# Optimization experiments

Measured on AMD Instinct MI355X. Metric: run time of the kernel, lower is better.

Reference implementation:

```python
import jax, jax.numpy as jnp
import numpy as np

B, T, F = 131072, 15, 12
H1, H2, CS = 64, 128, 96  # num_h1, num_h2, input_feature*8


def _lstm_cell(x, h, c, w_ih, w_hh, b_ih, b_hh):
    # torch.nn.LSTMCell gate order: i, f, g, o
    gates = x @ w_ih.T + h @ w_hh.T + b_ih + b_hh  # [B, 4H]
    i, f, g, o = jnp.split(gates, 4, axis=-1)
    i, f, o = jax.nn.sigmoid(i), jax.nn.sigmoid(f), jax.nn.sigmoid(o)
    g = jnp.tanh(g)
    c_new = f * c + i * g
    h_new = o * jnp.tanh(c_new)
    return h_new, c_new


def setup_inputs() -> dict:
    key = jax.random.key(0)
    ks = jax.random.split(key, 16)
    s = 0.05
    return {
        "input_seq": jax.random.normal(ks[0], (B, T, F), jnp.float32),
        "cell_state": jax.random.normal(ks[1], (B, CS), jnp.float32),
        "fc1_w": jax.random.normal(ks[2], (H1, CS), jnp.float32) * s,
        "fc1_b": jnp.zeros((H1,), jnp.float32),
        "fc2_w": jax.random.normal(ks[3], (H2, CS), jnp.float32) * s,
        "fc2_b": jnp.zeros((H2,), jnp.float32),
        "l0_w_ih": jax.random.normal(ks[4], (4 * H1, F), jnp.float32) * s,
        "l0_w_hh": jax.random.normal(ks[5], (4 * H1, H1), jnp.float32) * s,
        "l0_b_ih": jnp.zeros((4 * H1,), jnp.float32),
        "l0_b_hh": jnp.zeros((4 * H1,), jnp.float32),
        "l1_w_ih": jax.random.normal(ks[6], (4 * H2, H1), jnp.float32) * s,
        "l1_w_hh": jax.random.normal(ks[7], (4 * H2, H2), jnp.float32) * s,
        "l1_b_ih": jnp.zeros((4 * H2,), jnp.float32),
        "l1_b_hh": jnp.zeros((4 * H2,), jnp.float32),
        "d1_w": jax.random.normal(ks[8], (H1, H2), jnp.float32) * s,
        "d1_b": jnp.zeros((H1,), jnp.float32),
        "d2_w": jax.random.normal(ks[9], (1, H1), jnp.float32) * s,
        "d2_b": jnp.zeros((1,), jnp.float32),
    }


def reference(input_seq, cell_state, fc1_w, fc1_b, fc2_w, fc2_b,
              l0_w_ih, l0_w_hh, l0_b_ih, l0_b_hh,
              l1_w_ih, l1_w_hh, l1_b_ih, l1_b_hh,
              d1_w, d1_b, d2_w, d2_b):
    # dropout in eval mode (identity) for deterministic reference
    h0 = jnp.zeros((input_seq.shape[0], H1), input_seq.dtype)
    c0 = cell_state @ fc1_w.T + fc1_b
    h1 = jnp.zeros((input_seq.shape[0], H2), input_seq.dtype)
    c1 = cell_state @ fc2_w.T + fc2_b

    def step(carry, x_t):
        h0, c0, h1, c1 = carry
        h0n, c0_res = _lstm_cell(x_t, h0, c0, l0_w_ih, l0_w_hh, l0_b_ih, l0_b_hh)
        c0n = c0 + c0_res  # residual cell state
        h1n, c1_res = _lstm_cell(h0n, h1, c1, l1_w_ih, l1_w_hh, l1_b_ih, l1_b_hh)
        c1n = c1 + c1_res
        return (h0n, c0n, h1n, c1n), None

    xs = jnp.swapaxes(input_seq, 0, 1)  # [T, B, F]
    (h0, c0, h1, c1), _ = jax.lax.scan(step, (h0, c0, h1, c1), xs)
    pred = (h1 @ d1_w.T + d1_b) @ d2_w.T + d2_b  # [B, 1]
    return pred
```

## Files before the change

kernel.cpp:

```cpp
#include <hip/hip_runtime.h>


typedef float    f32x4 __attribute__((ext_vector_type(4)));
typedef _Float16 f16x8 __attribute__((ext_vector_type(8)));
typedef _Float16 f16x4 __attribute__((ext_vector_type(4)));

#define DEV static __device__ __forceinline__

DEV float fexp2(float x){ return __builtin_amdgcn_exp2f(x); }
DEV float frcp (float x){ return __builtin_amdgcn_rcpf(x); }

#define MFMA16(A,B,C) __builtin_amdgcn_mfma_f32_16x16x32_f16(A,B,C,0,0,0)

constexpr int T = 15, F = 12, CS = 96;
constexpr int R = 32;

constexpr int Q1OFF  = 0;
constexpr int Q0HOFF = 196608;
constexpr int Q0XOFF = 229376;
constexpr int QF2OFF = 245760;
constexpr int QF1OFF = 270336;

constexpr float NL2E = -1.44269504f, PL2E2 = 2.88539008f;

constexpr int OH0 = 0;
constexpr int OH1 = 8192;
constexpr int OX  = 24576;
constexpr int OKC = 28672;
constexpr int OWE = 31744;
constexpr int OWX = 32768;
constexpr int OC  = 49152;
constexpr int LDSB= 73728;

__global__ __launch_bounds__(64) void prequant(
    const float* __restrict__ fc1w, const float* __restrict__ fc2w,
    const float* __restrict__ w0i,  const float* __restrict__ w0h,
    const float* __restrict__ w1i,  const float* __restrict__ w1h,
    char* __restrict__ ws)
{
  const int r = blockIdx.x, j = threadIdx.x;
  auto put = [&](long off, float v){ *(_Float16*)(ws + off) = (_Float16)v; };
  if (r < 512){
    int n = r, lr = n & 15, wv = (n & 127) >> 4, g = n >> 7;
    #pragma unroll
    for (int c = 0; c < 3; ++c){
      int k = j + c*64;
      float v = (k < 64) ? w1i[n*64 + k] : w1h[n*128 + (k - 64)];
      int ks = k >> 5, lane = (((k >> 3) & 3) << 4) + lr, jj = k & 7;
      put(Q1OFF + ((long)(((wv*4+g)*6+ks)*64 + lane))*16 + jj*2, v);
    }
  } else if (r < 768){
    int n = r - 512, lr = n & 15, grp = (n & 63) >> 4, g = n >> 6;
    {
      int k = j;
      int ks = k >> 5, lane = (((k >> 3) & 3) << 4) + lr, jj = k & 7;
      put(Q0HOFF + ((long)(((grp*4+g)*2+ks)*64 + lane))*16 + jj*2, w0h[n*64 + k]);
    }
    if (j < 32){
      int k = j;
      int lane = (((k >> 3) & 3) << 4) + lr, jj = k & 7;
      float v = (k < 12) ? w0i[n*12 + k] : 0.f;
      put(Q0XOFF + ((long)((grp*4+g)*64 + lane))*16 + jj*2, v);
    }
  } else {
    bool t2 = (r < 896);
    int n = t2 ? (r - 768) : (r - 896);
    const float* fw = t2 ? fc2w : fc1w;
    long base = t2 ? QF2OFF : QF1OFF;
    int lr = n & 15, grp = n >> 4;
    #pragma unroll
    for (int c = 0; c < 2; ++c){
      int k = j + c*64;
      if (k < 96){
        int ks = k >> 5, lane = (((k >> 3) & 3) << 4) + lr, jj = k & 7;
        put(base + ((long)((grp*3+ks)*64 + lane))*16 + jj*2, fw[n*CS + k]);
      }
    }
  }
}

DEV float cellupd(float t0, float t1, float t2, float t3, float& c){
  float ei = fexp2(t0);
  float ef = fexp2(t1);
  float eg = fexp2(t2);
  float eo = fexp2(t3);
  float e1 = 1.f + ei, e2 = eg + 1.f, e3 = 1.f + ef;
  float m1 = e1 * e2;
  float num = fmaf(c, m1, (eg - 1.f) * e3);
  float tmp = num * frcp(m1 * e3);
  c += tmp;
  float tc = fminf(tmp, 12.0f);
  float ec = fexp2(tc * PL2E2);
  return (ec - 1.f) * frcp((1.f + eo) * (ec + 1.f));
}

__global__ __launch_bounds__(512, 2) void caurec(
    const float* __restrict__ x,    const float* __restrict__ cs,
    const float* __restrict__ fc1b, const float* __restrict__ fc2b,
    const float* __restrict__ b0i,  const float* __restrict__ b0h,
    const float* __restrict__ b1i,  const float* __restrict__ b1h,
    const float* __restrict__ d1w,  const float* __restrict__ d1b,
    const float* __restrict__ d2w,  const float* __restrict__ d2b,
    const char* __restrict__ ws,    float* __restrict__ out)
{
  __shared__ alignas(16) char L[LDSB];

  const int tid  = threadIdx.x;
  const int wave = tid >> 6, lane = tid & 63, lr = lane & 15, lg = lane >> 4;
  const int n0   = (wave & 3) * 16, mB0 = (wave >> 2) * 16, n1 = wave * 16;
  const int grp  = wave & 3;
  const int rowBase = blockIdx.x * R;
  const int sw8  = (lr & 7) << 4;

  const int rb0   = OH0 + lr*128 + ((lg*16) ^ sw8);
  const int rb0w  = rb0 + mB0*128;
  const int rb1   = OH1 + lr*256 + ((lg*16) ^ sw8);
  const int xrdb  = OX + (mB0 + lr)*64 + lg*16;
  const int kadC1 = OKC + wave*256 + lr*16;
  const int kadC0 = OKC + 2048 + grp*256 + lr*16;
  const int cst1  = OH1 + (lg*4)*256 + (((n1 + lr)*2) ^ ((lg & 1) << 6));
  const int cst0  = OH0 + (mB0 + lg*4)*128 + (((n0 + lr)*2) ^ ((lg & 1) << 6));
  const int owxb  = OWX + (grp*4)*1024 + lane*16;
  const int cbase = OC + tid*4;
  const int xr = tid/3, xq = tid - (tid/3)*3;
  const int xst = OX + xr*64 + xq*8;

  int zro = 0;

  {
    unsigned* W = (unsigned*)L;
    for (int i = tid; i < 3072; i += 512) W[1024 + i] = 0u;
    for (int i = tid; i < 1024; i += 512) W[6144 + i] = 0u;
  }
  __syncthreads();

  {
    int r = tid >> 4, cq = tid & 15;
    if (cq < 12){
      float4 v0 = *(const float4*)&cs[(size_t)(rowBase + r)*CS + cq*8];
      float4 v1 = *(const float4*)&cs[(size_t)(rowBase + r)*CS + cq*8 + 4];
      f16x8 V;
      V[0]=(_Float16)v0.x; V[1]=(_Float16)v0.y; V[2]=(_Float16)v0.z; V[3]=(_Float16)v0.w;
      V[4]=(_Float16)v1.x; V[5]=(_Float16)v1.y; V[6]=(_Float16)v1.z; V[7]=(_Float16)v1.w;
      int ad = OH1 + 8192 + r*256 + ((cq*16) ^ ((r & 7) << 4));
      *(f16x8*)(L + ad) = V;
    }
  }
  if (tid < 96){
    float4 v = *(const float4*)&x[((size_t)(rowBase + xr)*T + 0)*F + xq*4];
    f16x4 w; w[0]=(_Float16)v.x; w[1]=(_Float16)v.y; w[2]=(_Float16)v.z; w[3]=(_Float16)v.w;
    *(f16x4*)(L + xst) = w;
  }
  if (tid < 128){
    float s = 0.f;
    for (int a = 0; a < 64; ++a) s += d2w[a] * d1w[a*128 + tid];
    ((float*)(L + OWE))[tid] = s;
  } else if (tid == 128){
    float s = 0.f;
    for (int a = 0; a < 64; ++a) s += d2w[a] * d1b[a];
    ((float*)(L + OWE))[128] = s + d2b[0];
  }
  if (lg == 0){
    f32x4 c1k, c0k;
    #pragma unroll
    for (int g = 0; g < 4; ++g){
      float f = (g == 2) ? PL2E2 : NL2E;
      c1k[g] = f * (b1i[g*128 + n1 + lr] + b1h[g*128 + n1 + lr]);
      c0k[g] = f * (b0i[g*64  + n0 + lr] + b0h[g*64  + n0 + lr]);
    }
    *(f32x4*)(L + kadC1) = c1k;
    *(f32x4*)(L + kadC0) = c0k;
  }
  #pragma unroll
  for (int k = 0; k < 4; ++k){
    int i = tid + k*512;
    *(long*)(L + OWX + i*8) = *(const long*)(ws + Q0XOFF + i*8);
  }
  f16x8 WB1[4][6];
  #pragma unroll
  for (int g = 0; g < 4; ++g)
    #pragma unroll
    for (int ks = 0; ks < 6; ++ks)
      WB1[g][ks] = *(const f16x8*)(ws + Q1OFF + ((long)(((wave*4+g)*6+ks)*64 + lane))*16);
  __syncthreads();

  {
    const f32x4 Zf = {0.f,0.f,0.f,0.f};
    float bb2 = fc2b[n1 + lr];
    #pragma unroll
    for (int mt = 0; mt < 2; ++mt){
      f32x4 a = Zf;
      #pragma unroll
      for (int ks = 0; ks < 3; ++ks){
        f16x8 A = *(const f16x8*)(L + ((rb1 ^ (ks << 6)) + 8192 + mt*4096));
        f16x8 B = *(const f16x8*)(ws + QF2OFF + ((long)((wave*3+ks)*64 + lane))*16);
        a = MFMA16(A, B, a);
      }
      #pragma unroll
      for (int e = 0; e < 4; ++e)
        *(float*)(L + cbase + (mt*4 + e)*2048) = a[e] + bb2;
    }
    float bb1 = fc1b[n0 + lr];
    {
      f32x4 a = Zf;
      #pragma unroll
      for (int ks = 0; ks < 3; ++ks){
        f16x8 A = *(const f16x8*)(L + ((rb1 ^ (ks << 6)) + 8192 + mB0*256));
        f16x8 B = *(const f16x8*)(ws + QF1OFF + ((long)((grp*3+ks)*64 + lane))*16);
        a = MFMA16(A, B, a);
      }
      #pragma unroll
      for (int e = 0; e < 4; ++e)
        *(float*)(L + cbase + (8 + e)*2048) = a[e] + bb1;
    }
  }
  __syncthreads();

  auto l1_one = [&](int mt, int p8, int p16, int q16){
    const f32x4 Zf = {0.f,0.f,0.f,0.f};
    f32x4 kC = *(const f32x4*)(L + kadC1);
    f16x8 H = *(const f16x8*)(L + (rb0 + p8 + mt*2048));
    f32x4 a0 = MFMA16(H, WB1[0][0], Zf);
    f32x4 a1 = MFMA16(H, WB1[1][0], Zf);
    f32x4 a2 = MFMA16(H, WB1[2][0], Zf);
    f32x4 a3 = MFMA16(H, WB1[3][0], Zf);
    H = *(const f16x8*)(L + ((rb0 ^ 64) + p8 + mt*2048));
    a0 = MFMA16(H, WB1[0][1], a0); a1 = MFMA16(H, WB1[1][1], a1);
    a2 = MFMA16(H, WB1[2][1], a2); a3 = MFMA16(H, WB1[3][1], a3);
    #pragma unroll
    for (int ks = 0; ks < 4; ++ks){
      H = *(const f16x8*)(L + ((rb1 ^ (ks << 6)) + p16 + mt*4096));
      a0 = MFMA16(H, WB1[0][2+ks], a0); a1 = MFMA16(H, WB1[1][2+ks], a1);
      a2 = MFMA16(H, WB1[2][2+ks], a2); a3 = MFMA16(H, WB1[3][2+ks], a3);
    }
    const int sb = cst1 + q16 + mt*4096;
    #pragma unroll
    for (int e = 0; e < 4; ++e){
      float t0 = fmaf(a0[e], NL2E,  kC[0]);
      float t1 = fmaf(a1[e], NL2E,  kC[1]);
      float t2 = fmaf(a2[e], PL2E2, kC[2]);
      float t3 = fmaf(a3[e], NL2E,  kC[3]);
      float cc = *(const float*)(L + cbase + (mt*4 + e)*2048);
      float h = cellupd(t0, t1, t2, t3, cc);
      *(float*)(L + cbase + (mt*4 + e)*2048) = cc;
      *(_Float16*)(L + ((sb + e*256) ^ (e << 4))) = (_Float16)h;
    }
  };

  auto l0_one = [&](int p8, int px, int q8){
    const f32x4 Zf = {0.f,0.f,0.f,0.f};
    f32x4 kC = *(const f32x4*)(L + kadC0);
    f16x8 X  = *(const f16x8*)(L + (xrdb + px));
    f16x8 H0 = *(const f16x8*)(L + (rb0w + p8));
    f16x8 H1 = *(const f16x8*)(L + ((rb0w ^ 64) + p8));
    const char* whp = ws + (long)(Q0HOFF + zro) + (long)(grp*8)*1024 + (long)lane*16;
    f32x4 acc[4];
    #pragma unroll
    for (int g = 0; g < 4; ++g){
      f16x8 W0 = *(const f16x8*)(whp + (g*2+0)*1024);
      f16x8 W1 = *(const f16x8*)(whp + (g*2+1)*1024);
      f16x8 Wx = *(const f16x8*)(L + owxb + g*1024);
      f32x4 a = MFMA16(H0, W0, Zf);
      a = MFMA16(H1, W1, a);
      a = MFMA16(X,  Wx, a);
      acc[g] = a;
    }
    const int sb = cst0 + q8;
    #pragma unroll
    for (int e = 0; e < 4; ++e){
      float t0 = fmaf(acc[0][e], NL2E,  kC[0]);
      float t1 = fmaf(acc[1][e], NL2E,  kC[1]);
      float t2 = fmaf(acc[2][e], PL2E2, kC[2]);
      float t3 = fmaf(acc[3][e], NL2E,  kC[3]);
      float cc = *(const float*)(L + cbase + (8 + e)*2048);
      float h = cellupd(t0, t1, t2, t3, cc);
      *(float*)(L + cbase + (8 + e)*2048) = cc;
      *(_Float16*)(L + ((sb + e*128) ^ (e << 4))) = (_Float16)h;
    }
  };

  {
    float4 xv; const bool doX = tid < 96;
    if (doX) xv = *(const float4*)&x[((size_t)(rowBase + xr)*T + 1)*F + xq*4];
    l0_one(4096, 0, 0);
    if (doX){
      f16x4 w; w[0]=(_Float16)xv.x; w[1]=(_Float16)xv.y; w[2]=(_Float16)xv.z; w[3]=(_Float16)xv.w;
      *(f16x4*)(L + xst + 2048) = w;
    }
    __syncthreads();
  }

  for (int j = 0; j < 7; ++j){
    asm volatile("" : "+v"(zro));
    {
      float4 xv; const bool doX = tid < 96;
      if (doX) xv = *(const float4*)&x[((size_t)(rowBase + xr)*T + (2*j + 2))*F + xq*4];
      l1_one(0, 0, 0, 8192);
      l1_one(1, 0, 0, 8192);
      l0_one(0, 2048, 4096);
      if (doX){
        f16x4 w; w[0]=(_Float16)xv.x; w[1]=(_Float16)xv.y; w[2]=(_Float16)xv.z; w[3]=(_Float16)xv.w;
        *(f16x4*)(L + xst) = w;
      }
      __syncthreads();
    }
    {
      float4 xv; const bool doX = (j < 6) && (tid < 96);
      if (doX) xv = *(const float4*)&x[((size_t)(rowBase + xr)*T + (2*j + 3))*F + xq*4];
      l1_one(0, 4096, 8192, 0);
      l1_one(1, 4096, 8192, 0);
      l0_one(4096, 0, 0);
      if (doX){
        f16x4 w; w[0]=(_Float16)xv.x; w[1]=(_Float16)xv.y; w[2]=(_Float16)xv.z; w[3]=(_Float16)xv.w;
        *(f16x4*)(L + xst + 2048) = w;
      }
      __syncthreads();
    }
  }

  {
    l1_one(0, 0, 0, 8192);
    l1_one(1, 0, 0, 8192);
    __syncthreads();
  }

  {
    int r = tid >> 4, s = tid & 15;
    const float* wE = (const float*)(L + OWE);
    float sum = 0.f;
    #pragma unroll
    for (int cc = 0; cc < 8; ++cc){
      int c = s*8 + cc;
      const char* pe = L + OH1 + 8192 + r*256 + ((c*2) ^ ((r & 7) << 4));
      sum += (float)(*(const _Float16*)pe) * wE[c];
    }
    sum += __shfl_down(sum, 8);
    sum += __shfl_down(sum, 4);
    sum += __shfl_down(sum, 2);
    sum += __shfl_down(sum, 1);
    if (s == 0) out[rowBase + r] = sum + wE[128];
  }
}

extern "C" void kernel_launch(void* const* d_in, const int* in_sizes, int n_in,
                              void* d_out, int out_size, void* d_ws, size_t ws_size,
                              hipStream_t stream) {
  const float* x    = (const float*)d_in[0];
  const float* cs   = (const float*)d_in[1];
  const float* fc1w = (const float*)d_in[2];
  const float* fc1b = (const float*)d_in[3];
  const float* fc2w = (const float*)d_in[4];
  const float* fc2b = (const float*)d_in[5];
  const float* w0i  = (const float*)d_in[6];
  const float* w0h  = (const float*)d_in[7];
  const float* b0i  = (const float*)d_in[8];
  const float* b0h  = (const float*)d_in[9];
  const float* w1i  = (const float*)d_in[10];
  const float* w1h  = (const float*)d_in[11];
  const float* b1i  = (const float*)d_in[12];
  const float* b1h  = (const float*)d_in[13];
  const float* d1w  = (const float*)d_in[14];
  const float* d1b  = (const float*)d_in[15];
  const float* d2w  = (const float*)d_in[16];
  const float* d2b  = (const float*)d_in[17];

  char* ws = (char*)d_ws;
  prequant<<<960, 64, 0, stream>>>(fc1w, fc2w, w0i, w0h, w1i, w1h, ws);

  const int Btot = in_sizes[0] / (T * F);
  const int grid = Btot / R;
  caurec<<<grid, 512, 0, stream>>>(x, cs, fc1b, fc2b, b0i, b0h, b1i, b1h,
                                   d1w, d1b, d2w, d2b, ws, (float*)d_out);
}
```

Before: 694.4 us.

## Cut layer-1 weight register footprint by streaming two K-slices from global memory

Result: slower. 790.0 us (+13.8%).

```diff
diff --git a/kernel.cpp b/kernel.cpp
--- a/kernel.cpp
+++ b/kernel.cpp
@@ -176,11 +176,11 @@
     int i = tid + k*512;
     *(long*)(L + OWX + i*8) = *(const long*)(ws + Q0XOFF + i*8);
   }
-  f16x8 WB1[4][6];
+  f16x8 WB1[4][4];
   #pragma unroll
   for (int g = 0; g < 4; ++g)
     #pragma unroll
-    for (int ks = 0; ks < 6; ++ks)
+    for (int ks = 0; ks < 4; ++ks)
       WB1[g][ks] = *(const f16x8*)(ws + Q1OFF + ((long)(((wave*4+g)*6+ks)*64 + lane))*16);
   __syncthreads();
 
@@ -219,29 +219,42 @@
   auto l1_one = [&](int mt, int p8, int p16, int q16){
     const f32x4 Zf = {0.f,0.f,0.f,0.f};
     f32x4 kC = *(const f32x4*)(L + kadC1);
-    f16x8 H = *(const f16x8*)(L + (rb0 + p8 + mt*2048));
-    f32x4 a0 = MFMA16(H, WB1[0][0], Zf);
-    f32x4 a1 = MFMA16(H, WB1[1][0], Zf);
-    f32x4 a2 = MFMA16(H, WB1[2][0], Zf);
-    f32x4 a3 = MFMA16(H, WB1[3][0], Zf);
-    H = *(const f16x8*)(L + ((rb0 ^ 64) + p8 + mt*2048));
-    a0 = MFMA16(H, WB1[0][1], a0); a1 = MFMA16(H, WB1[1][1], a1);
-    a2 = MFMA16(H, WB1[2][1], a2); a3 = MFMA16(H, WB1[3][1], a3);
-    #pragma unroll
-    for (int ks = 0; ks < 4; ++ks){
-      H = *(const f16x8*)(L + ((rb1 ^ (ks << 6)) + p16 + mt*4096));
-      a0 = MFMA16(H, WB1[0][2+ks], a0); a1 = MFMA16(H, WB1[1][2+ks], a1);
-      a2 = MFMA16(H, WB1[2][2+ks], a2); a3 = MFMA16(H, WB1[3][2+ks], a3);
+    const char* w1p = ws + (long)(Q1OFF + zro) + (long)lane*16;
+    float tg0[4], tg1[4], tg2[4], tg3[4];
+    #pragma unroll
+    for (int gp = 0; gp < 2; ++gp){
+      const int ga = 2*gp, gb = 2*gp + 1;
+      f16x8 Wa4 = *(const f16x8*)(w1p + (long)(((wave*4+ga)*6+4)*64)*16);
+      f16x8 Wa5 = *(const f16x8*)(w1p + (long)(((wave*4+ga)*6+5)*64)*16);
+      f16x8 Wb4 = *(const f16x8*)(w1p + (long)(((wave*4+gb)*6+4)*64)*16);
+      f16x8 Wb5 = *(const f16x8*)(w1p + (long)(((wave*4+gb)*6+5)*64)*16);
+      f16x8 H = *(const f16x8*)(L + (rb0 + p8 + mt*2048));
+      f32x4 aA = MFMA16(H, WB1[ga][0], Zf);
+      f32x4 aB = MFMA16(H, WB1[gb][0], Zf);
+      H = *(const f16x8*)(L + ((rb0 ^ 64) + p8 + mt*2048));
+      aA = MFMA16(H, WB1[ga][1], aA); aB = MFMA16(H, WB1[gb][1], aB);
+      H = *(const f16x8*)(L + (rb1 + p16 + mt*4096));
+      aA = MFMA16(H, WB1[ga][2], aA); aB = MFMA16(H, WB1[gb][2], aB);
+      H = *(const f16x8*)(L + ((rb1 ^ 64) + p16 + mt*4096));
+      aA = MFMA16(H, WB1[ga][3], aA); aB = MFMA16(H, WB1[gb][3], aB);
+      H = *(const f16x8*)(L + ((rb1 ^ 128) + p16 + mt*4096));
+      aA = MFMA16(H, Wa4, aA); aB = MFMA16(H, Wb4, aB);
+      H = *(const f16x8*)(L + ((rb1 ^ 192) + p16 + mt*4096));
+      aA = MFMA16(H, Wa5, aA); aB = MFMA16(H, Wb5, aB);
+      float fa = (ga == 2) ? PL2E2 : NL2E;
+      #pragma unroll
+      for (int e = 0; e < 4; ++e){
+        float tA = fmaf(aA[e], fa,   kC[ga]);
+        float tB = fmaf(aB[e], NL2E, kC[gb]);
+        if (gp == 0){ tg0[e] = tA; tg1[e] = tB; }
+        else        { tg2[e] = tA; tg3[e] = tB; }
+      }
     }
     const int sb = cst1 + q16 + mt*4096;
     #pragma unroll
     for (int e = 0; e < 4; ++e){
-      float t0 = fmaf(a0[e], NL2E,  kC[0]);
-      float t1 = fmaf(a1[e], NL2E,  kC[1]);
-      float t2 = fmaf(a2[e], PL2E2, kC[2]);
-      float t3 = fmaf(a3[e], NL2E,  kC[3]);
       float cc = *(const float*)(L + cbase + (mt*4 + e)*2048);
-      float h = cellupd(t0, t1, t2, t3, cc);
+      float h = cellupd(tg0[e], tg1[e], tg2[e], tg3[e], cc);
       *(float*)(L + cbase + (mt*4 + e)*2048) = cc;
       *(_Float16*)(L + ((sb + e*256) ^ (e << 4))) = (_Float16)h;
     }
@@ -254,7 +267,7 @@
     f16x8 H0 = *(const f16x8*)(L + (rb0w + p8));
     f16x8 H1 = *(const f16x8*)(L + ((rb0w ^ 64) + p8));
     const char* whp = ws + (long)(Q0HOFF + zro) + (long)(grp*8)*1024 + (long)lane*16;
-    f32x4 acc[4];
+    float tg0[4], tg1[4], tg2[4], tg3[4];
     #pragma unroll
     for (int g = 0; g < 4; ++g){
       f16x8 W0 = *(const f16x8*)(whp + (g*2+0)*1024);
@@ -263,62 +276,56 @@
       f32x4 a = MFMA16(H0, W0, Zf);
       a = MFMA16(H1, W1, a);
       a = MFMA16(X,  Wx, a);
-      acc[g] = a;
+      float f = (g == 2) ? PL2E2 : NL2E;
+      float* tg = (g==0)?tg0:(g==1)?tg1:(g==2)?tg2:tg3;
+      #pragma unroll
+      for (int e = 0; e < 4; ++e) tg[e] = fmaf(a[e], f, kC[g]);
     }
     const int sb = cst0 + q8;
     #pragma unroll
     for (int e = 0; e < 4; ++e){
-      float t0 = fmaf(acc[0][e], NL2E,  kC[0]);
-      float t1 = fmaf(acc[1][e], NL2E,  kC[1]);
-      float t2 = fmaf(acc[2][e], PL2E2, kC[2]);
-      float t3 = fmaf(acc[3][e], NL2E,  kC[3]);
       float cc = *(const float*)(L + cbase + (8 + e)*2048);
-      float h = cellupd(t0, t1, t2, t3, cc);
+      float h = cellupd(tg0[e], tg1[e], tg2[e], tg3[e], cc);
       *(float*)(L + cbase + (8 + e)*2048) = cc;
       *(_Float16*)(L + ((sb + e*128) ^ (e << 4))) = (_Float16)h;
     }
   };
 
-  {
-    float4 xv; const bool doX = tid < 96;
-    if (doX) xv = *(const float4*)&x[((size_t)(rowBase + xr)*T + 1)*F + xq*4];
+  auto stageX = [&](int t, int ofs){
+    if (tid < 96){
+      float4 v = *(const float4*)&x[((size_t)(rowBase + xr)*T + t)*F + xq*4];
+      f16x4 w; w[0]=(_Float16)v.x; w[1]=(_Float16)v.y; w[2]=(_Float16)v.z; w[3]=(_Float16)v.w;
+      *(f16x4*)(L + xst + ofs) = w;
+    }
+  };
+
+  {
     l0_one(4096, 0, 0);
-    if (doX){
-      f16x4 w; w[0]=(_Float16)xv.x; w[1]=(_Float16)xv.y; w[2]=(_Float16)xv.z; w[3]=(_Float16)xv.w;
-      *(f16x4*)(L + xst + 2048) = w;
-    }
+    stageX(1, 2048);
     __syncthreads();
   }
 
   for (int j = 0; j < 7; ++j){
-    asm volatile("" : "+v"(zro));
     {
-      float4 xv; const bool doX = tid < 96;
-      if (doX) xv = *(const float4*)&x[((size_t)(rowBase + xr)*T + (2*j + 2))*F + xq*4];
+      asm volatile("" : "+v"(zro));
       l1_one(0, 0, 0, 8192);
       l1_one(1, 0, 0, 8192);
       l0_one(0, 2048, 4096);
-      if (doX){
-        f16x4 w; w[0]=(_Float16)xv.x; w[1]=(_Float16)xv.y; w[2]=(_Float16)xv.z; w[3]=(_Float16)xv.w;
-        *(f16x4*)(L + xst) = w;
-      }
+      stageX(2*j + 2, 0);
       __syncthreads();
     }
     {
-      float4 xv; const bool doX = (j < 6) && (tid < 96);
-      if (doX) xv = *(const float4*)&x[((size_t)(rowBase + xr)*T + (2*j + 3))*F + xq*4];
+      asm volatile("" : "+v"(zro));
       l1_one(0, 4096, 8192, 0);
       l1_one(1, 4096, 8192, 0);
       l0_one(4096, 0, 0);
-      if (doX){
-        f16x4 w; w[0]=(_Float16)xv.x; w[1]=(_Float16)xv.y; w[2]=(_Float16)xv.z; w[3]=(_Float16)xv.w;
-        *(f16x4*)(L + xst + 2048) = w;
-      }
+      if (j < 6) stageX(2*j + 3, 2048);
       __syncthreads();
     }
   }
 
   {
+    asm volatile("" : "+v"(zro));
     l1_one(0, 0, 0, 8192);
     l1_one(1, 0, 0, 8192);
     __syncthreads();
```
